# Optimization experiments

Measured on AMD Instinct MI355X. Metric: run time of the kernel, lower is better.

Reference implementation:

```python
import jax, jax.numpy as jnp
import numpy as np

C = 6      # in_channel (forced by the module's own shape constraints)
MID = 3    # in_channel // 2
EPS = 1e-5


def setup_inputs() -> dict:
    key = jax.random.key(0)
    ks = jax.random.split(key, 16)
    B, N, NC, L = 2, 32768, 3, 2048
    w = lambda k, shape: jax.random.normal(k, shape, jnp.float32) * 0.2
    return {
        "x": jax.random.normal(ks[0], (B, C, N), jnp.float32),
        "curves": jax.random.normal(ks[1], (B, C, NC, L), jnp.float32),
        "Wa": w(ks[2], (MID, C)),    # conva   (Conv1d C->MID, k=1, no bias)
        "Wav": w(ks[3], (MID, C)),   # conva_v
        "Wb": w(ks[4], (MID, C)),    # convb
        "Wbv": w(ks[5], (MID, C)),   # convb_v
        "Wc": w(ks[6], (MID, C)),    # convc
        "Wd": w(ks[7], (C, 2 * MID)),  # convd Conv1d 2*MID -> C
        "bn_gamma": jnp.ones((C,), jnp.float32),
        "bn_beta": jnp.zeros((C,), jnp.float32),
        "Watt": w(ks[8], (C,)),      # line_conv_att Conv2d C->1, k=1
        "ln_gamma": jnp.ones((2 * MID,), jnp.float32),
        "ln_beta": jnp.zeros((2 * MID,), jnp.float32),
        "Wpl": w(ks[9], (MID, 3)),   # p_l Conv1d 3->MID (with bias)
        "bpl": w(ks[10], (MID,)),
        "Wpn": w(ks[11], (MID, 3)),  # p_n Conv1d 3->MID (with bias)
        "bpn": w(ks[12], (MID,)),
    }


def reference(x, curves, Wa, Wav, Wb, Wbv, Wc, Wd, bn_gamma, bn_beta,
              Watt, ln_gamma, ln_beta, Wpl, bpl, Wpn, bpn):
    # p, curve = curves  (tensor unpack along dim 0)
    p = curves[0]                                        # [C, 3, L]
    # p_l / p_n: Conv1d(3, MID) with p treated as batch=C, channels=3
    pl = jnp.einsum('bkl,mk->bml', p, Wpl) + bpl[None, :, None]   # [C, MID, L]
    p_l = pl.mean(axis=-1)                               # [C, MID]
    pn = jnp.einsum('bkl,mk->bml', p, Wpn) + bpn[None, :, None]   # [C, MID, L]
    p_n = pn.mean(axis=-2)                               # [C, L]

    # line attention over curves
    att = jnp.einsum('bcnl,c->bnl', curves, Watt)[:, None, :, :]  # [B,1,3,L]
    curver_inter = (curves * jax.nn.softmax(att, axis=-1)).sum(axis=-1)  # [B,C,3]
    curves_intra = (curves * jax.nn.softmax(att, axis=-2)).sum(axis=-2)  # [B,C,L]

    gi = curver_inter + p_l                              # [B,C,3] + [C,3(MID)]
    ga = curves_intra + p_n                              # [B,C,L] + [C,L]
    k_inter = jnp.einsum('bcn,mc->bmn', gi, Wa)          # [B,MID,3]
    v_inter = jnp.einsum('bcn,mc->bnm', gi, Wav)         # [B,3,MID]
    k_intra = jnp.einsum('bcl,mc->bml', ga, Wb)          # [B,MID,L]
    v_intra = jnp.einsum('bcl,mc->blm', ga, Wbv)         # [B,L,MID]

    q = jnp.einsum('bcn,mc->bnm', x, Wc)                 # [B,N,MID]
    scale = jnp.sqrt(jnp.float32(q.shape[-1]))           # sqrt(MID)

    att_inter = jax.nn.softmax(jnp.einsum('bnm,bmk->bnk', q, k_inter) / scale, axis=-1)
    feature_inter = jnp.einsum('bnk,bkm->bnm', att_inter, v_inter)   # [B,N,MID]
    att_intra = jax.nn.softmax(jnp.einsum('bnm,bml->bnl', q, k_intra) / scale, axis=-1)
    feature_intra = jnp.einsum('bnl,blm->bnm', att_intra, v_intra)   # [B,N,MID]

    cf = jnp.concatenate([feature_inter, feature_intra], axis=-1)    # [B,N,2*MID]
    mu = cf.mean(axis=-1, keepdims=True)
    var = ((cf - mu) ** 2).mean(axis=-1, keepdims=True)
    cf = (cf - mu) * jax.lax.rsqrt(var + EPS) * ln_gamma + ln_beta   # LayerNorm
    cf = jnp.swapaxes(cf, 1, 2)                                      # [B,2*MID,N]

    y = jnp.einsum('bcn,oc->bon', cf, Wd)                # Conv1d 2*MID -> C
    # BatchNorm1d (training-mode batch statistics over (B, N))
    bm = y.mean(axis=(0, 2), keepdims=True)
    bv = ((y - bm) ** 2).mean(axis=(0, 2), keepdims=True)
    y = (y - bm) * jax.lax.rsqrt(bv + EPS) * bn_gamma[None, :, None] + bn_beta[None, :, None]

    out = x + y
    return jnp.where(out >= 0, out, 0.2 * out)           # LeakyReLU(0.2)
```

## Files before the change

### kernel.cpp

```cpp
#include <hip/hip_runtime.h>
#include <math.h>

#define N_PTS 32768
#define LL    2048

#define KT_U      0
#define VT_U      8192
#define PART_OFF  16384
#define MS_OFF    28672
#define W_OFF     28684
#define CS_OFF    28720
#define PBKM_OFF  28738
#define BNS_OFF   28762
#define BNB_OFF   28768

typedef __fp16 h2    __attribute__((ext_vector_type(2)));
typedef __fp16 f16x4 __attribute__((ext_vector_type(4)));
typedef float  f32x4 __attribute__((ext_vector_type(4)));

__device__ __forceinline__ unsigned h2_bits(h2 h){
  union { h2 h; unsigned u; } x; x.h = h; return x.u;
}
__device__ __forceinline__ float wave_reduce_sum(float v){
  #pragma unroll
  for (int off = 32; off; off >>= 1) v += __shfl_xor(v, off, 64);
  return v;
}
__device__ __forceinline__ float wave_reduce_max(float v){
  #pragma unroll
  for (int off = 32; off; off >>= 1) v = fmaxf(v, __shfl_xor(v, off, 64));
  return v;
}

__global__ __launch_bounds__(256)
void prep_kernel(const float* __restrict__ curves, const float* __restrict__ Watt,
                 const float* __restrict__ Wb,  const float* __restrict__ Wbv,
                 const float* __restrict__ Wpn, const float* __restrict__ bpn,
                 float* __restrict__ ws)
{
  const int blk = blockIdx.x, tid = threadIdx.x;
  const int lane = tid & 63, wid = tid >> 6;
  __shared__ float sred[4 * 13];
  __shared__ float msh;

  float watt[6];
  #pragma unroll
  for (int c = 0; c < 6; c++) watt[c] = Watt[c];

  if (blk < 6) {
    const int b = blk / 3, nc = blk % 3;
    const float* cb = curves + b * 18 * LL;
    float av[8], pm = -1e30f;
    #pragma unroll
    for (int k = 0; k < 8; k++) {
      const int l = tid + k * 256;
      float s = 0.f;
      #pragma unroll
      for (int c = 0; c < 6; c++) s = fmaf(cb[(c * 3 + nc) * LL + l], watt[c], s);
      av[k] = s; pm = fmaxf(pm, s);
    }
    pm = wave_reduce_max(pm);
    if (lane == 0) sred[wid] = pm;
    __syncthreads();
    if (tid == 0) msh = fmaxf(fmaxf(sred[0], sred[1]), fmaxf(sred[2], sred[3]));
    __syncthreads();
    const float m = msh;

    float vals[13];
    #pragma unroll
    for (int j = 0; j < 13; j++) vals[j] = 0.f;
    #pragma unroll
    for (int k = 0; k < 8; k++) {
      const int l = tid + k * 256;
      float e = __expf(av[k] - m);
      vals[0] += e;
      #pragma unroll
      for (int c = 0; c < 6; c++) {
        float v = cb[(c * 3 + nc) * LL + l];
        vals[1 + c] = fmaf(v, e, vals[1 + c]);
        if (b == 0) vals[7 + c] += v;
      }
    }
    __syncthreads();
    #pragma unroll
    for (int j = 0; j < 13; j++) vals[j] = wave_reduce_sum(vals[j]);
    if (lane == 0) { for (int j = 0; j < 13; j++) sred[wid * 13 + j] = vals[j]; }
    __syncthreads();
    if (tid == 0) {
      ws[MS_OFF + blk * 2] = m;
      for (int j = 0; j < 13; j++) {
        float s = sred[j] + sred[13 + j] + sred[26 + j] + sred[39 + j];
        if (j == 0) ws[MS_OFF + blk * 2 + 1] = s;
        else if (j < 7) ws[W_OFF + blk * 6 + (j - 1)] = s;
        else if (b == 0) ws[CS_OFF + nc * 6 + (j - 7)] = s;
      }
    }
  } else {
    const int idx = (blk - 6) * 256 + tid;
    const int b = idx >> 10, pp = idx & 1023, l = pp * 2;
    const float* cb = curves + b * 18 * LL;

    float2 cv[6][3], pv[6][3];
    #pragma unroll
    for (int c = 0; c < 6; c++)
      #pragma unroll
      for (int nc = 0; nc < 3; nc++) {
        cv[c][nc] = *(const float2*)&cb[(c * 3 + nc) * LL + l];
        pv[c][nc] = *(const float2*)&curves[(c * 3 + nc) * LL + l];
      }
    float a[3][2];
    #pragma unroll
    for (int nc = 0; nc < 3; nc++) {
      float sx = 0.f, sy = 0.f;
      #pragma unroll
      for (int c = 0; c < 6; c++) {
        sx = fmaf(cv[c][nc].x, watt[c], sx);
        sy = fmaf(cv[c][nc].y, watt[c], sy);
      }
      a[nc][0] = sx; a[nc][1] = sy;
    }

    float wb_r[18], wbv_r[18];
    #pragma unroll
    for (int i = 0; i < 18; i++) { wb_r[i] = Wb[i]; wbv_r[i] = Wbv[i]; }
    const float wn0 = (Wpn[0] + Wpn[3] + Wpn[6]) * (1.f / 3.f);
    const float wn1 = (Wpn[1] + Wpn[4] + Wpn[7]) * (1.f / 3.f);
    const float wn2 = (Wpn[2] + Wpn[5] + Wpn[8]) * (1.f / 3.f);
    const float bnb = (bpn[0] + bpn[1] + bpn[2]) * (1.f / 3.f);

    float kk[2][3], vv[2][3], km[3] = {0.f, 0.f, 0.f};
    #pragma unroll
    for (int e = 0; e < 2; e++) {
      float a0 = a[0][e], a1 = a[1][e], a2 = a[2][e];
      float mm = fmaxf(fmaxf(a0, a1), a2);
      float e0 = __expf(a0 - mm), e1 = __expf(a1 - mm), e2 = __expf(a2 - mm);
      float r = 1.f / (e0 + e1 + e2);
      float ga[6];
      #pragma unroll
      for (int c = 0; c < 6; c++) {
        float c0 = e ? cv[c][0].y : cv[c][0].x;
        float c1 = e ? cv[c][1].y : cv[c][1].x;
        float c2 = e ? cv[c][2].y : cv[c][2].x;
        float p0 = e ? pv[c][0].y : pv[c][0].x;
        float p1 = e ? pv[c][1].y : pv[c][1].x;
        float p2 = e ? pv[c][2].y : pv[c][2].x;
        float intra = (c0 * e0 + c1 * e1 + c2 * e2) * r;
        float pn = p0 * wn0 + p1 * wn1 + p2 * wn2 + bnb;
        ga[c] = intra + pn;
      }
      float k0 = 0, k1 = 0, k2 = 0, v0 = 0, v1 = 0, v2 = 0;
      #pragma unroll
      for (int c = 0; c < 6; c++) {
        k0 += wb_r[c] * ga[c];  k1 += wb_r[6 + c] * ga[c];  k2 += wb_r[12 + c] * ga[c];
        v0 += wbv_r[c] * ga[c]; v1 += wbv_r[6 + c] * ga[c]; v2 += wbv_r[12 + c] * ga[c];
      }
      kk[e][0] = k0; kk[e][1] = k1; kk[e][2] = k2;
      vv[e][0] = v0; vv[e][1] = v1; vv[e][2] = v2;
      km[0] = fmaxf(km[0], fabsf(k0));
      km[1] = fmaxf(km[1], fabsf(k1));
      km[2] = fmaxf(km[2], fabsf(k2));
    }
    unsigned* ktg = (unsigned*)ws + KT_U + b * 4096;
    ktg[4 * pp + 0] = h2_bits(__builtin_amdgcn_cvt_pkrtz(kk[0][0], kk[0][1]));
    ktg[4 * pp + 1] = h2_bits(__builtin_amdgcn_cvt_pkrtz(kk[0][2], 0.f));
    ktg[4 * pp + 2] = h2_bits(__builtin_amdgcn_cvt_pkrtz(kk[1][0], kk[1][1]));
    ktg[4 * pp + 3] = h2_bits(__builtin_amdgcn_cvt_pkrtz(kk[1][2], 0.f));
    unsigned* vtg = (unsigned*)ws + VT_U + b * 4096;
    vtg[0 * 1024 + pp] = h2_bits(__builtin_amdgcn_cvt_pkrtz(vv[0][0], vv[1][0]));
    vtg[1 * 1024 + pp] = h2_bits(__builtin_amdgcn_cvt_pkrtz(vv[0][1], vv[1][1]));
    vtg[2 * 1024 + pp] = h2_bits(__builtin_amdgcn_cvt_pkrtz(vv[0][2], vv[1][2]));
    vtg[3 * 1024 + pp] = h2_bits(__builtin_amdgcn_cvt_pkrtz(1.f, 1.f));

    #pragma unroll
    for (int j = 0; j < 3; j++) km[j] = wave_reduce_max(km[j]);
    if (lane == 0) { for (int j = 0; j < 3; j++) sred[wid * 3 + j] = km[j]; }
    __syncthreads();
    if (tid == 0) {
      for (int j = 0; j < 3; j++)
        ws[PBKM_OFF + (blk - 6) * 3 + j] =
          fmaxf(fmaxf(sred[j], sred[3 + j]), fmaxf(sred[6 + j], sred[9 + j]));
    }
  }
}

__global__ __launch_bounds__(256, 4)
void attn_kernel(const float* __restrict__ x,  const float* __restrict__ Wc,
                 const float* __restrict__ Wd, const float* __restrict__ lng,
                 const float* __restrict__ lnb,
                 const float* __restrict__ Wa, const float* __restrict__ Wav,
                 const float* __restrict__ Wpl, const float* __restrict__ bpl,
                 float* __restrict__ ws, float* __restrict__ yout)
{
  __shared__ __align__(16) unsigned kt[4224];
  __shared__ __align__(16) unsigned vt[4224];
  __shared__ float4 cross[2][64];
  __shared__ float gis[18], kis[9], vis[9];
  const int tid  = threadIdx.x, blk = blockIdx.x;
  const int lane = tid & 63, w = tid >> 6;
  const int col  = lane & 15, hi4 = lane >> 4;
  const int rp   = w >> 1, kh = w & 1;
  const int rbase = blk * 64;
  const int b    = rbase >> 15;
  const int nb   = rbase & (N_PTS - 1);

  {
    const uint4* ktg = (const uint4*)((const unsigned*)ws + KT_U + b * 4096);
    uint4* kt4 = (uint4*)kt;
    for (int i = tid; i < 1024; i += 256) kt4[i] = ktg[i];
    const uint2* vtg2 = (const uint2*)((const unsigned*)ws + VT_U + b * 4096);
    for (int i = tid; i < 2048; i += 256) {
      int pl = i >> 9, off = (i & 511) << 1;
      *(uint2*)&vt[pl * 1028 + off] = vtg2[i];
    }
    if (tid < 2) { kt[4096 + tid] = 0; vt[4112 + tid] = 0; }
  }
  if (tid < 18) {
    int c = tid / 3, m = tid % 3;
    float pl_ = bpl[m];
    #pragma unroll
    for (int k = 0; k < 3; k++)
      pl_ = fmaf(Wpl[m * 3 + k], ws[CS_OFF + k * 6 + c] * (1.f / LL), pl_);
    gis[c * 3 + m] = ws[W_OFF + (b * 3 + m) * 6 + c] / ws[MS_OFF + (b * 3 + m) * 2 + 1] + pl_;
  }
  __syncthreads();
  if (tid < 9) {
    int m = tid / 3, k = tid % 3;
    float s1 = 0.f, s2 = 0.f;
    #pragma unroll
    for (int c = 0; c < 6; c++) {
      float g = gis[c * 3 + k];
      s1 = fmaf(Wa [m * 6 + c], g, s1);
      s2 = fmaf(Wav[m * 6 + c], g, s2);
    }
    kis[m * 3 + k] = s1; vis[k * 3 + m] = s2;
  }

  float km0 = 0.f, km1 = 0.f, km2 = 0.f;
  #pragma unroll
  for (int s = 0; s < 4; s++) {
    const float* pk = ws + PBKM_OFF + (b * 4 + s) * 3;
    km0 = fmaxf(km0, pk[0]); km1 = fmaxf(km1, pk[1]); km2 = fmaxf(km2, pk[2]);
  }

  const int nA = nb + rp * 32 + col, nBr = nA + 16;
  const float* xb = x + (size_t)b * 6 * N_PTS;
  float q0A = 0, q1A = 0, q2A = 0, q0B = 0, q1B = 0, q2B = 0;
  #pragma unroll
  for (int c = 0; c < 6; c++) {
    float xvA = xb[c * N_PTS + nA], xvB = xb[c * N_PTS + nBr];
    q0A = fmaf(xvA, Wc[c], q0A); q1A = fmaf(xvA, Wc[6 + c], q1A); q2A = fmaf(xvA, Wc[12 + c], q2A);
    q0B = fmaf(xvB, Wc[c], q0B); q1B = fmaf(xvB, Wc[6 + c], q1B); q2B = fmaf(xvB, Wc[12 + c], q2B);
  }
  const float KS = 1.4426950408889634f * 0.57735026918962576f;
  q0A *= KS; q1A *= KS; q2A *= KS; q0B *= KS; q1B *= KS; q2B *= KS;
  const float MpA = fabsf(q0A) * km0 + fabsf(q1A) * km1 + fabsf(q2A) * km2;
  const float MpB = fabsf(q0B) * km0 + fabsf(q1B) * km1 + fabsf(q2B) * km2;

  union U2 { uint2 u; f16x4 h; };
  U2 qbA, qbB;
  qbA.u.x = qbA.u.y = qbB.u.x = qbB.u.y = 0;
  if (hi4 == 0) {
    qbA.u.x = h2_bits(__builtin_amdgcn_cvt_pkrtz(q0A, q1A));
    qbA.u.y = h2_bits(__builtin_amdgcn_cvt_pkrtz(q2A, 0.f));
    qbB.u.x = h2_bits(__builtin_amdgcn_cvt_pkrtz(q0B, q1B));
    qbB.u.y = h2_bits(__builtin_amdgcn_cvt_pkrtz(q2B, 0.f));
  }
  f32x4 cbA = { -MpA, -MpA, -MpA, -MpA };
  f32x4 cbB = { -MpB, -MpB, -MpB, -MpB };
  f32x4 aA0 = {0,0,0,0}, aA1 = {0,0,0,0}, aB0 = {0,0,0,0}, aB1 = {0,0,0,0};

  unsigned ki_ = (hi4 == 0) ? (unsigned)(kh * 2048 + col * 2) : 4096u;
  const unsigned kd = (hi4 == 0) ? 32u : 0u;
  unsigned vi_ = (col < 4) ? (unsigned)(col * 1028 + kh * 512 + 2 * hi4) : 4112u;
  const unsigned vd = (col < 4) ? 8u : 0u;

  U2 Kc, Vc, Kn, Vn;
  Kc.u = *(const uint2*)&kt[ki_];
  Vc.u = *(const uint2*)&vt[vi_];
  ki_ += kd; vi_ += vd;
  Kn.u = *(const uint2*)&kt[ki_];
  Vn.u = *(const uint2*)&vt[vi_];
  f32x4 sAc = __builtin_amdgcn_mfma_f32_16x16x16f16(Kc.h, qbA.h, cbA, 0, 0, 0);
  f32x4 sBc = __builtin_amdgcn_mfma_f32_16x16x16f16(Kc.h, qbB.h, cbB, 0, 0, 0);

  #pragma unroll 2
  for (int i = 0; i < 62; i++) {
    f32x4 sAn = __builtin_amdgcn_mfma_f32_16x16x16f16(Kn.h, qbA.h, cbA, 0, 0, 0);
    f32x4 sBn = __builtin_amdgcn_mfma_f32_16x16x16f16(Kn.h, qbB.h, cbB, 0, 0, 0);
    ki_ += kd;
    Kn.u = *(const uint2*)&kt[ki_];
    float eA0 = __builtin_amdgcn_exp2f(sAc[0]);
    float eA1 = __builtin_amdgcn_exp2f(sAc[1]);
    float eA2 = __builtin_amdgcn_exp2f(sAc[2]);
    float eA3 = __builtin_amdgcn_exp2f(sAc[3]);
    float eB0 = __builtin_amdgcn_exp2f(sBc[0]);
    float eB1 = __builtin_amdgcn_exp2f(sBc[1]);
    float eB2 = __builtin_amdgcn_exp2f(sBc[2]);
    float eB3 = __builtin_amdgcn_exp2f(sBc[3]);
    U2 PA, PB;
    PA.u.x = h2_bits(__builtin_amdgcn_cvt_pkrtz(eA0, eA1));
    PA.u.y = h2_bits(__builtin_amdgcn_cvt_pkrtz(eA2, eA3));
    PB.u.x = h2_bits(__builtin_amdgcn_cvt_pkrtz(eB0, eB1));
    PB.u.y = h2_bits(__builtin_amdgcn_cvt_pkrtz(eB2, eB3));
    if (i & 1) {
      aA1 = __builtin_amdgcn_mfma_f32_16x16x16f16(Vc.h, PA.h, aA1, 0, 0, 0);
      aB1 = __builtin_amdgcn_mfma_f32_16x16x16f16(Vc.h, PB.h, aB1, 0, 0, 0);
    } else {
      aA0 = __builtin_amdgcn_mfma_f32_16x16x16f16(Vc.h, PA.h, aA0, 0, 0, 0);
      aB0 = __builtin_amdgcn_mfma_f32_16x16x16f16(Vc.h, PB.h, aB0, 0, 0, 0);
    }
    Vc = Vn;
    vi_ += vd;
    Vn.u = *(const uint2*)&vt[vi_];
    sAc = sAn; sBc = sBn;
  }
  {
    f32x4 sAn = __builtin_amdgcn_mfma_f32_16x16x16f16(Kn.h, qbA.h, cbA, 0, 0, 0);
    f32x4 sBn = __builtin_amdgcn_mfma_f32_16x16x16f16(Kn.h, qbB.h, cbB, 0, 0, 0);
    #pragma unroll
    for (int e = 0; e < 2; e++) {
      float e0 = __builtin_amdgcn_exp2f(sAc[0]);
      float e1 = __builtin_amdgcn_exp2f(sAc[1]);
      float e2 = __builtin_amdgcn_exp2f(sAc[2]);
      float e3 = __builtin_amdgcn_exp2f(sAc[3]);
      float f0 = __builtin_amdgcn_exp2f(sBc[0]);
      float f1 = __builtin_amdgcn_exp2f(sBc[1]);
      float f2 = __builtin_amdgcn_exp2f(sBc[2]);
      float f3 = __builtin_amdgcn_exp2f(sBc[3]);
      U2 PA, PB;
      PA.u.x = h2_bits(__builtin_amdgcn_cvt_pkrtz(e0, e1));
      PA.u.y = h2_bits(__builtin_amdgcn_cvt_pkrtz(e2, e3));
      PB.u.x = h2_bits(__builtin_amdgcn_cvt_pkrtz(f0, f1));
      PB.u.y = h2_bits(__builtin_amdgcn_cvt_pkrtz(f2, f3));
      if (e == 0) {
        aA0 = __builtin_amdgcn_mfma_f32_16x16x16f16(Vc.h, PA.h, aA0, 0, 0, 0);
        aB0 = __builtin_amdgcn_mfma_f32_16x16x16f16(Vc.h, PB.h, aB0, 0, 0, 0);
        Vc = Vn; sAc = sAn; sBc = sBn;
      } else {
        aA1 = __builtin_amdgcn_mfma_f32_16x16x16f16(Vc.h, PA.h, aA1, 0, 0, 0);
        aB1 = __builtin_amdgcn_mfma_f32_16x16x16f16(Vc.h, PB.h, aB1, 0, 0, 0);
      }
    }
  }

  if (hi4 == 0) {
    cross[kh][rp * 32 + col] =
      make_float4(aA0[0] + aA1[0], aA0[1] + aA1[1], aA0[2] + aA1[2], aA0[3] + aA1[3]);
    cross[kh][rp * 32 + 16 + col] =
      make_float4(aB0[0] + aB1[0], aB0[1] + aB1[1], aB0[2] + aB1[2], aB0[3] + aB1[3]);
  }
  __syncthreads();

  if (tid < 64) {
    const int ri = tid, n = nb + ri;
    float4 c0 = cross[0][ri], c1 = cross[1][ri];
    float w0 = c0.x + c1.x, w1 = c0.y + c1.y, w2 = c0.z + c1.z, dd = c0.w + c1.w;

    float a0 = 0, a1 = 0, a2 = 0;
    #pragma unroll
    for (int c = 0; c < 6; c++) {
      float xv = xb[c * N_PTS + n];
      a0 = fmaf(xv, Wc[c], a0); a1 = fmaf(xv, Wc[6 + c], a1); a2 = fmaf(xv, Wc[12 + c], a2);
    }
    a0 *= KS; a1 *= KS; a2 *= KS;

    float sk0 = a0 * kis[0] + a1 * kis[3] + a2 * kis[6];
    float sk1 = a0 * kis[1] + a1 * kis[4] + a2 * kis[7];
    float sk2 = a0 * kis[2] + a1 * kis[5] + a2 * kis[8];
    float mm  = fmaxf(fmaxf(sk0, sk1), sk2);
    float e0 = __builtin_amdgcn_exp2f(sk0 - mm);
    float e1 = __builtin_amdgcn_exp2f(sk1 - mm);
    float e2 = __builtin_amdgcn_exp2f(sk2 - mm);
    float rs = 1.f / (e0 + e1 + e2);
    float fi0 = (e0 * vis[0] + e1 * vis[3] + e2 * vis[6]) * rs;
    float fi1 = (e0 * vis[1] + e1 * vis[4] + e2 * vis[7]) * rs;
    float fi2 = (e0 * vis[2] + e1 * vis[5] + e2 * vis[8]) * rs;
    float rinv = 1.f / dd;
    float cf[6] = { fi0, fi1, fi2, w0 * rinv, w1 * rinv, w2 * rinv };

    float mu = (cf[0] + cf[1] + cf[2] + cf[3] + cf[4] + cf[5]) * (1.f / 6.f);
    float var = 0.f;
    #pragma unroll
    for (int i = 0; i < 6; i++) { float t = cf[i] - mu; var += t * t; }
    var *= (1.f / 6.f);
    float rn = rsqrtf(var + 1e-5f);
    float cfn[6];
    #pragma unroll
    for (int i = 0; i < 6; i++) cfn[i] = (cf[i] - mu) * rn * lng[i] + lnb[i];

    float v12[12];
    #pragma unroll
    for (int o = 0; o < 6; o++) {
      float s = 0.f;
      #pragma unroll
      for (int c = 0; c < 6; c++) s += Wd[o * 6 + c] * cfn[c];
      yout[(size_t)b * (6 * N_PTS) + o * N_PTS + n] = s;
      v12[o] = s; v12[6 + o] = s * s;
    }
    #pragma unroll
    for (int j = 0; j < 12; j++) v12[j] = wave_reduce_sum(v12[j]);
    if (tid == 0) {
      float* part = ws + PART_OFF + blk * 12;
      for (int j = 0; j < 12; j++) part[j] = v12[j];
    }
  }
}

__global__ __launch_bounds__(256)
void final_kernel(const float* __restrict__ x,
                  const float* __restrict__ bng, const float* __restrict__ bnbt,
                  const float* __restrict__ ws, float* __restrict__ out)
{
  __shared__ float cp[48];
  __shared__ float sc_s[6], sh_s[6];
  const int tid = threadIdx.x, blk = blockIdx.x;
  const int lane = tid & 63, wid = tid >> 6;
  const float* part = ws + PART_OFF;

  float v[12];
  #pragma unroll
  for (int j = 0; j < 12; j++) v[j] = 0.f;
  #pragma unroll
  for (int k = 0; k < 4; k++) {
    const float* p = part + (tid * 4 + k) * 12;
    #pragma unroll
    for (int j = 0; j < 12; j++) v[j] += p[j];
  }
  #pragma unroll
  for (int j = 0; j < 12; j++) v[j] = wave_reduce_sum(v[j]);
  if (lane == 0) { for (int j = 0; j < 12; j++) cp[wid * 12 + j] = v[j]; }
  __syncthreads();
  if (tid < 6) {
    const float inv = 1.f / 65536.f;
    float s1 = cp[tid] + cp[12 + tid] + cp[24 + tid] + cp[36 + tid];
    float s2 = cp[6 + tid] + cp[18 + tid] + cp[30 + tid] + cp[42 + tid];
    float mean = s1 * inv;
    float varr = s2 * inv - mean * mean;
    float sc = bng[tid] * rsqrtf(varr + 1e-5f);
    sc_s[tid] = sc;
    sh_s[tid] = bnbt[tid] - mean * sc;
  }
  __syncthreads();

  const int base = blk * 1024 + tid * 4;
  const int ch = (base >> 15) % 6;
  const float sc = sc_s[ch], sh = sh_s[ch];
  float4 o = *(float4*)&out[base];
  float4 xx = *(const float4*)&x[base];
  float r[4] = { o.x * sc + sh + xx.x, o.y * sc + sh + xx.y,
                 o.z * sc + sh + xx.z, o.w * sc + sh + xx.w };
  #pragma unroll
  for (int j = 0; j < 4; j++) r[j] = r[j] >= 0.f ? r[j] : 0.2f * r[j];
  *(float4*)&out[base] = make_float4(r[0], r[1], r[2], r[3]);
}

extern "C" void kernel_launch(void* const* d_in, const int* in_sizes, int n_in,
                              void* d_out, int out_size, void* d_ws, size_t ws_size,
                              hipStream_t stream)
{
  const float* x      = (const float*)d_in[0];
  const float* curves = (const float*)d_in[1];
  const float* Wa     = (const float*)d_in[2];
  const float* Wav    = (const float*)d_in[3];
  const float* Wb     = (const float*)d_in[4];
  const float* Wbv    = (const float*)d_in[5];
  const float* Wc     = (const float*)d_in[6];
  const float* Wd     = (const float*)d_in[7];
  const float* bng    = (const float*)d_in[8];
  const float* bnbt   = (const float*)d_in[9];
  const float* Watt   = (const float*)d_in[10];
  const float* lng    = (const float*)d_in[11];
  const float* lnbt   = (const float*)d_in[12];
  const float* Wpl    = (const float*)d_in[13];
  const float* bpl    = (const float*)d_in[14];
  const float* Wpn    = (const float*)d_in[15];
  const float* bpn    = (const float*)d_in[16];
  float* out = (float*)d_out;
  float* ws  = (float*)d_ws;

  prep_kernel<<<14, 256, 0, stream>>>(curves, Watt, Wb, Wbv, Wpn, bpn, ws);
  attn_kernel<<<1024, 256, 0, stream>>>(x, Wc, Wd, lng, lnbt,
                                        Wa, Wav, Wpl, bpl, ws, out);
  final_kernel<<<384, 256, 0, stream>>>(x, bng, bnbt, ws, out);
}
```

Measured before the change: 34.38 us.

## Use 1024-thread attention blocks sharing K/V tiles with MFMA-ready layout

The attention kernel now launches 256 blocks of 1024 threads, each covering 256 query rows, so the per-batch K and V tiles staged in LDS are shared by four times as many rows. The prep kernel writes K and V to global memory in a swizzled layout that matches the MFMA operand order. This lets the attention loop load 128-bit chunks covering two MFMA steps at once, and the LDS fill becomes one uint4 per thread. The BN partial sums are combined inside the block, so the final kernel reads one partial per thread. In exchange there are fewer blocks than the GPU's workgroup slots, a larger block-wide sync, and the software pipelining that overlapped the QK and PV MFMAs is dropped.

```diff
diff --git a/kernel.cpp b/kernel.cpp
--- a/kernel.cpp
+++ b/kernel.cpp
@@ -160,16 +160,24 @@
       km[1] = fmaxf(km[1], fabsf(k1));
       km[2] = fmaxf(km[2], fabsf(k2));
     }
+
     unsigned* ktg = (unsigned*)ws + KT_U + b * 4096;
-    ktg[4 * pp + 0] = h2_bits(__builtin_amdgcn_cvt_pkrtz(kk[0][0], kk[0][1]));
-    ktg[4 * pp + 1] = h2_bits(__builtin_amdgcn_cvt_pkrtz(kk[0][2], 0.f));
-    ktg[4 * pp + 2] = h2_bits(__builtin_amdgcn_cvt_pkrtz(kk[1][0], kk[1][1]));
-    ktg[4 * pp + 3] = h2_bits(__builtin_amdgcn_cvt_pkrtz(kk[1][2], 0.f));
-    unsigned* vtg = (unsigned*)ws + VT_U + b * 4096;
-    vtg[0 * 1024 + pp] = h2_bits(__builtin_amdgcn_cvt_pkrtz(vv[0][0], vv[1][0]));
-    vtg[1 * 1024 + pp] = h2_bits(__builtin_amdgcn_cvt_pkrtz(vv[0][1], vv[1][1]));
-    vtg[2 * 1024 + pp] = h2_bits(__builtin_amdgcn_cvt_pkrtz(vv[0][2], vv[1][2]));
-    vtg[3 * 1024 + pp] = h2_bits(__builtin_amdgcn_cvt_pkrtz(1.f, 1.f));
+    #pragma unroll
+    for (int e = 0; e < 2; e++) {
+      const int k = l + e;
+      const int idxk = (k >> 5) * 64 + (k & 15) * 4 + (((k >> 4) & 1) << 1);
+      ktg[idxk]     = h2_bits(__builtin_amdgcn_cvt_pkrtz(kk[e][0], kk[e][1]));
+      ktg[idxk + 1] = h2_bits(__builtin_amdgcn_cvt_pkrtz(kk[e][2], 0.f));
+    }
+    {
+      unsigned* vtg = (unsigned*)ws + VT_U + b * 4096;
+      const int cp = pp >> 4, c2 = (pp >> 3) & 1, p = (2 * pp) & 15;
+      const int base = cp * 64 + (p >> 2) * 4 + c2 * 2 + ((p >> 1) & 1);
+      vtg[base]      = h2_bits(__builtin_amdgcn_cvt_pkrtz(vv[0][0], vv[1][0]));
+      vtg[base + 16] = h2_bits(__builtin_amdgcn_cvt_pkrtz(vv[0][1], vv[1][1]));
+      vtg[base + 32] = h2_bits(__builtin_amdgcn_cvt_pkrtz(vv[0][2], vv[1][2]));
+      vtg[base + 48] = h2_bits(__builtin_amdgcn_cvt_pkrtz(1.f, 1.f));
+    }
 
     #pragma unroll
     for (int j = 0; j < 3; j++) km[j] = wave_reduce_max(km[j]);
@@ -183,7 +191,7 @@
   }
 }
 
-__global__ __launch_bounds__(256, 4)
+__global__ __launch_bounds__(1024, 4)
 void attn_kernel(const float* __restrict__ x,  const float* __restrict__ Wc,
                  const float* __restrict__ Wd, const float* __restrict__ lng,
                  const float* __restrict__ lnb,
@@ -193,26 +201,23 @@
 {
   __shared__ __align__(16) unsigned kt[4224];
   __shared__ __align__(16) unsigned vt[4224];
-  __shared__ float4 cross[2][64];
+  __shared__ float4 cross[4][2][64];
+  __shared__ float cp[16 * 12];
   __shared__ float gis[18], kis[9], vis[9];
   const int tid  = threadIdx.x, blk = blockIdx.x;
   const int lane = tid & 63, w = tid >> 6;
   const int col  = lane & 15, hi4 = lane >> 4;
-  const int rp   = w >> 1, kh = w & 1;
-  const int rbase = blk * 64;
+  const int rg   = w >> 2, rp = (w >> 1) & 1, kh = w & 1;
+  const int rbase = blk * 256;
   const int b    = rbase >> 15;
   const int nb   = rbase & (N_PTS - 1);
 
   {
     const uint4* ktg = (const uint4*)((const unsigned*)ws + KT_U + b * 4096);
-    uint4* kt4 = (uint4*)kt;
-    for (int i = tid; i < 1024; i += 256) kt4[i] = ktg[i];
-    const uint2* vtg2 = (const uint2*)((const unsigned*)ws + VT_U + b * 4096);
-    for (int i = tid; i < 2048; i += 256) {
-      int pl = i >> 9, off = (i & 511) << 1;
-      *(uint2*)&vt[pl * 1028 + off] = vtg2[i];
-    }
-    if (tid < 2) { kt[4096 + tid] = 0; vt[4112 + tid] = 0; }
+    const uint4* vtg = (const uint4*)((const unsigned*)ws + VT_U + b * 4096);
+    ((uint4*)kt)[tid] = ktg[tid];
+    ((uint4*)vt)[tid] = vtg[tid];
+    if (tid < 8) { kt[4096 + tid] = 0; vt[4096 + tid] = 0; }
   }
   if (tid < 18) {
     int c = tid / 3, m = tid % 3;
@@ -242,7 +247,7 @@
     km0 = fmaxf(km0, pk[0]); km1 = fmaxf(km1, pk[1]); km2 = fmaxf(km2, pk[2]);
   }
 
-  const int nA = nb + rp * 32 + col, nBr = nA + 16;
+  const int nA = nb + rg * 64 + rp * 32 + col, nBr = nA + 16;
   const float* xb = x + (size_t)b * 6 * N_PTS;
   float q0A = 0, q1A = 0, q2A = 0, q0B = 0, q1B = 0, q2B = 0;
   #pragma unroll
@@ -257,6 +262,7 @@
   const float MpB = fabsf(q0B) * km0 + fabsf(q1B) * km1 + fabsf(q2B) * km2;
 
   union U2 { uint2 u; f16x4 h; };
+  union U4 { uint4 q; f16x4 h[2]; };
   U2 qbA, qbB;
   qbA.u.x = qbA.u.y = qbB.u.x = qbB.u.y = 0;
   if (hi4 == 0) {
@@ -269,91 +275,81 @@
   f32x4 cbB = { -MpB, -MpB, -MpB, -MpB };
   f32x4 aA0 = {0,0,0,0}, aA1 = {0,0,0,0}, aB0 = {0,0,0,0}, aB1 = {0,0,0,0};
 
-  unsigned ki_ = (hi4 == 0) ? (unsigned)(kh * 2048 + col * 2) : 4096u;
-  const unsigned kd = (hi4 == 0) ? 32u : 0u;
-  unsigned vi_ = (col < 4) ? (unsigned)(col * 1028 + kh * 512 + 2 * hi4) : 4112u;
-  const unsigned vd = (col < 4) ? 8u : 0u;
-
-  U2 Kc, Vc, Kn, Vn;
-  Kc.u = *(const uint2*)&kt[ki_];
-  Vc.u = *(const uint2*)&vt[vi_];
-  ki_ += kd; vi_ += vd;
-  Kn.u = *(const uint2*)&kt[ki_];
-  Vn.u = *(const uint2*)&vt[vi_];
-  f32x4 sAc = __builtin_amdgcn_mfma_f32_16x16x16f16(Kc.h, qbA.h, cbA, 0, 0, 0);
-  f32x4 sBc = __builtin_amdgcn_mfma_f32_16x16x16f16(Kc.h, qbB.h, cbB, 0, 0, 0);
-
-  #pragma unroll 2
-  for (int i = 0; i < 62; i++) {
-    f32x4 sAn = __builtin_amdgcn_mfma_f32_16x16x16f16(Kn.h, qbA.h, cbA, 0, 0, 0);
-    f32x4 sBn = __builtin_amdgcn_mfma_f32_16x16x16f16(Kn.h, qbB.h, cbB, 0, 0, 0);
-    ki_ += kd;
-    Kn.u = *(const uint2*)&kt[ki_];
-    float eA0 = __builtin_amdgcn_exp2f(sAc[0]);
-    float eA1 = __builtin_amdgcn_exp2f(sAc[1]);
-    float eA2 = __builtin_amdgcn_exp2f(sAc[2]);
-    float eA3 = __builtin_amdgcn_exp2f(sAc[3]);
-    float eB0 = __builtin_amdgcn_exp2f(sBc[0]);
-    float eB1 = __builtin_amdgcn_exp2f(sBc[1]);
-    float eB2 = __builtin_amdgcn_exp2f(sBc[2]);
-    float eB3 = __builtin_amdgcn_exp2f(sBc[3]);
+  unsigned ki_ = (hi4 == 0) ? (unsigned)(kh * 2048 + col * 4) : 4096u;
+  const unsigned kd = (hi4 == 0) ? 64u : 0u;
+  unsigned vi_ = (col < 4) ? (unsigned)(kh * 2048 + col * 16 + hi4 * 4) : 4096u;
+  const unsigned vd = (col < 4) ? 64u : 0u;
+
+  __syncthreads();
+
+  U4 Kc, Vc;
+  Kc.q = *(const uint4*)&kt[ki_];
+  Vc.q = *(const uint4*)&vt[vi_];
+
+  for (int i = 0; i < 32; i++) {
+    ki_ += kd; vi_ += vd;
+    U4 Kn, Vn;
+    Kn.q = *(const uint4*)&kt[ki_];
+    Vn.q = *(const uint4*)&vt[vi_];
+
+    f32x4 s0A = __builtin_amdgcn_mfma_f32_16x16x16f16(Kc.h[0], qbA.h, cbA, 0, 0, 0);
+    f32x4 s0B = __builtin_amdgcn_mfma_f32_16x16x16f16(Kc.h[0], qbB.h, cbB, 0, 0, 0);
+    f32x4 s1A = __builtin_amdgcn_mfma_f32_16x16x16f16(Kc.h[1], qbA.h, cbA, 0, 0, 0);
+    f32x4 s1B = __builtin_amdgcn_mfma_f32_16x16x16f16(Kc.h[1], qbB.h, cbB, 0, 0, 0);
+
     U2 PA, PB;
-    PA.u.x = h2_bits(__builtin_amdgcn_cvt_pkrtz(eA0, eA1));
-    PA.u.y = h2_bits(__builtin_amdgcn_cvt_pkrtz(eA2, eA3));
-    PB.u.x = h2_bits(__builtin_amdgcn_cvt_pkrtz(eB0, eB1));
-    PB.u.y = h2_bits(__builtin_amdgcn_cvt_pkrtz(eB2, eB3));
-    if (i & 1) {
-      aA1 = __builtin_amdgcn_mfma_f32_16x16x16f16(Vc.h, PA.h, aA1, 0, 0, 0);
-      aB1 = __builtin_amdgcn_mfma_f32_16x16x16f16(Vc.h, PB.h, aB1, 0, 0, 0);
-    } else {
-      aA0 = __builtin_amdgcn_mfma_f32_16x16x16f16(Vc.h, PA.h, aA0, 0, 0, 0);
-      aB0 = __builtin_amdgcn_mfma_f32_16x16x16f16(Vc.h, PB.h, aB0, 0, 0, 0);
-    }
-    Vc = Vn;
-    vi_ += vd;
-    Vn.u = *(const uint2*)&vt[vi_];
-    sAc = sAn; sBc = sBn;
-  }
-  {
-    f32x4 sAn = __builtin_amdgcn_mfma_f32_16x16x16f16(Kn.h, qbA.h, cbA, 0, 0, 0);
-    f32x4 sBn = __builtin_amdgcn_mfma_f32_16x16x16f16(Kn.h, qbB.h, cbB, 0, 0, 0);
-    #pragma unroll
-    for (int e = 0; e < 2; e++) {
-      float e0 = __builtin_amdgcn_exp2f(sAc[0]);
-      float e1 = __builtin_amdgcn_exp2f(sAc[1]);
-      float e2 = __builtin_amdgcn_exp2f(sAc[2]);
-      float e3 = __builtin_amdgcn_exp2f(sAc[3]);
-      float f0 = __builtin_amdgcn_exp2f(sBc[0]);
-      float f1 = __builtin_amdgcn_exp2f(sBc[1]);
-      float f2 = __builtin_amdgcn_exp2f(sBc[2]);
-      float f3 = __builtin_amdgcn_exp2f(sBc[3]);
-      U2 PA, PB;
+    {
+      float e0 = __builtin_amdgcn_exp2f(s0A[0]);
+      float e1 = __builtin_amdgcn_exp2f(s0A[1]);
+      float e2 = __builtin_amdgcn_exp2f(s0A[2]);
+      float e3 = __builtin_amdgcn_exp2f(s0A[3]);
+      float f0 = __builtin_amdgcn_exp2f(s0B[0]);
+      float f1 = __builtin_amdgcn_exp2f(s0B[1]);
+      float f2 = __builtin_amdgcn_exp2f(s0B[2]);
+      float f3 = __builtin_amdgcn_exp2f(s0B[3]);
       PA.u.x = h2_bits(__builtin_amdgcn_cvt_pkrtz(e0, e1));
       PA.u.y = h2_bits(__builtin_amdgcn_cvt_pkrtz(e2, e3));
       PB.u.x = h2_bits(__builtin_amdgcn_cvt_pkrtz(f0, f1));
       PB.u.y = h2_bits(__builtin_amdgcn_cvt_pkrtz(f2, f3));
-      if (e == 0) {
-        aA0 = __builtin_amdgcn_mfma_f32_16x16x16f16(Vc.h, PA.h, aA0, 0, 0, 0);
-        aB0 = __builtin_amdgcn_mfma_f32_16x16x16f16(Vc.h, PB.h, aB0, 0, 0, 0);
-        Vc = Vn; sAc = sAn; sBc = sBn;
-      } else {
-        aA1 = __builtin_amdgcn_mfma_f32_16x16x16f16(Vc.h, PA.h, aA1, 0, 0, 0);
-        aB1 = __builtin_amdgcn_mfma_f32_16x16x16f16(Vc.h, PB.h, aB1, 0, 0, 0);
-      }
-    }
+    }
+    aA0 = __builtin_amdgcn_mfma_f32_16x16x16f16(Vc.h[0], PA.h, aA0, 0, 0, 0);
+    aB0 = __builtin_amdgcn_mfma_f32_16x16x16f16(Vc.h[0], PB.h, aB0, 0, 0, 0);
+    {
+      float e0 = __builtin_amdgcn_exp2f(s1A[0]);
+      float e1 = __builtin_amdgcn_exp2f(s1A[1]);
+      float e2 = __builtin_amdgcn_exp2f(s1A[2]);
+      float e3 = __builtin_amdgcn_exp2f(s1A[3]);
+      float f0 = __builtin_amdgcn_exp2f(s1B[0]);
+      float f1 = __builtin_amdgcn_exp2f(s1B[1]);
+      float f2 = __builtin_amdgcn_exp2f(s1B[2]);
+      float f3 = __builtin_amdgcn_exp2f(s1B[3]);
+      PA.u.x = h2_bits(__builtin_amdgcn_cvt_pkrtz(e0, e1));
+      PA.u.y = h2_bits(__builtin_amdgcn_cvt_pkrtz(e2, e3));
+      PB.u.x = h2_bits(__builtin_amdgcn_cvt_pkrtz(f0, f1));
+      PB.u.y = h2_bits(__builtin_amdgcn_cvt_pkrtz(f2, f3));
+    }
+    aA1 = __builtin_amdgcn_mfma_f32_16x16x16f16(Vc.h[1], PA.h, aA1, 0, 0, 0);
+    aB1 = __builtin_amdgcn_mfma_f32_16x16x16f16(Vc.h[1], PB.h, aB1, 0, 0, 0);
+
+    Kc = Kn; Vc = Vn;
   }
 
   if (hi4 == 0) {
-    cross[kh][rp * 32 + col] =
+    cross[rg][kh][rp * 32 + col] =
       make_float4(aA0[0] + aA1[0], aA0[1] + aA1[1], aA0[2] + aA1[2], aA0[3] + aA1[3]);
-    cross[kh][rp * 32 + 16 + col] =
+    cross[rg][kh][rp * 32 + 16 + col] =
       make_float4(aB0[0] + aB1[0], aB0[1] + aB1[1], aB0[2] + aB1[2], aB0[3] + aB1[3]);
   }
   __syncthreads();
 
-  if (tid < 64) {
-    const int ri = tid, n = nb + ri;
-    float4 c0 = cross[0][ri], c1 = cross[1][ri];
+  float v12[12];
+  #pragma unroll
+  for (int j = 0; j < 12; j++) v12[j] = 0.f;
+
+  if (tid < 256) {
+    const int trg = tid >> 6, ri = tid & 63;
+    const int n = nb + trg * 64 + ri;
+    float4 c0 = cross[trg][0][ri], c1 = cross[trg][1][ri];
     float w0 = c0.x + c1.x, w1 = c0.y + c1.y, w2 = c0.z + c1.z, dd = c0.w + c1.w;
 
     float a0 = 0, a1 = 0, a2 = 0;
@@ -388,7 +384,6 @@
     #pragma unroll
     for (int i = 0; i < 6; i++) cfn[i] = (cf[i] - mu) * rn * lng[i] + lnb[i];
 
-    float v12[12];
     #pragma unroll
     for (int o = 0; o < 6; o++) {
       float s = 0.f;
@@ -397,12 +392,16 @@
       yout[(size_t)b * (6 * N_PTS) + o * N_PTS + n] = s;
       v12[o] = s; v12[6 + o] = s * s;
     }
-    #pragma unroll
-    for (int j = 0; j < 12; j++) v12[j] = wave_reduce_sum(v12[j]);
-    if (tid == 0) {
-      float* part = ws + PART_OFF + blk * 12;
-      for (int j = 0; j < 12; j++) part[j] = v12[j];
-    }
+  }
+
+  #pragma unroll
+  for (int j = 0; j < 12; j++) v12[j] = wave_reduce_sum(v12[j]);
+  if (lane == 0) { for (int j = 0; j < 12; j++) cp[w * 12 + j] = v12[j]; }
+  __syncthreads();
+  if (tid == 0) {
+    float* part = ws + PART_OFF + blk * 12;
+    for (int j = 0; j < 12; j++)
+      part[j] = cp[j] + cp[12 + j] + cp[24 + j] + cp[36 + j];
   }
 }
 
@@ -419,13 +418,7 @@
 
   float v[12];
   #pragma unroll
-  for (int j = 0; j < 12; j++) v[j] = 0.f;
-  #pragma unroll
-  for (int k = 0; k < 4; k++) {
-    const float* p = part + (tid * 4 + k) * 12;
-    #pragma unroll
-    for (int j = 0; j < 12; j++) v[j] += p[j];
-  }
+  for (int j = 0; j < 12; j++) v[j] = part[tid * 12 + j];
   #pragma unroll
   for (int j = 0; j < 12; j++) v[j] = wave_reduce_sum(v[j]);
   if (lane == 0) { for (int j = 0; j < 12; j++) cp[wid * 12 + j] = v[j]; }
@@ -479,7 +472,7 @@
   float* ws  = (float*)d_ws;
 
   prep_kernel<<<14, 256, 0, stream>>>(curves, Watt, Wb, Wbv, Wpn, bpn, ws);
-  attn_kernel<<<1024, 256, 0, stream>>>(x, Wc, Wd, lng, lnbt,
+  attn_kernel<<<256, 1024, 0, stream>>>(x, Wc, Wd, lng, lnbt,
                                         Wa, Wav, Wpl, bpl, ws, out);
   final_kernel<<<384, 256, 0, stream>>>(x, bng, bnbt, ws, out);
 }
```

Result: faster. 33.63 us (-2.2%).
